# Kernel optimization log

Measured on AMD Instinct MI355X. Metric: run time of the kernel, lower is better.

Reference implementation:

```python
import jax, jax.numpy as jnp
import numpy as np

MAXHD = 100.0
MAXV = 40.0
LSTM_UNITS = 20
IN_DIM = 12


def setup_inputs() -> dict:
    key = jax.random.key(0)
    ks = jax.random.split(key, 10)
    nveh, nt = 8192, 512
    leadfol_inputs = jax.random.normal(ks[0], (nveh, nt, IN_DIM), dtype=jnp.float32)
    true_traj = jax.random.normal(ks[1], (nveh, nt), dtype=jnp.float32)
    hidden_states = jnp.zeros((2, nveh, LSTM_UNITS), dtype=jnp.float32)
    s = 0.1
    # LSTM kernel/recurrent kernel/bias (keras gate order: i, f, c, o)
    W_k = jax.random.normal(ks[2], (IN_DIM, 4 * LSTM_UNITS), dtype=jnp.float32) * s
    W_r = jax.random.normal(ks[3], (LSTM_UNITS, 4 * LSTM_UNITS), dtype=jnp.float32) * s
    b_l = jnp.zeros((4 * LSTM_UNITS,), dtype=jnp.float32)
    # dense (10, relu) and lc_actions (3)
    W_d = jax.random.normal(ks[4], (LSTM_UNITS, 10), dtype=jnp.float32) * s
    b_d = jnp.zeros((10,), dtype=jnp.float32)
    W_lc = jax.random.normal(ks[5], (10, 3), dtype=jnp.float32) * s
    b_lc = jnp.zeros((3,), dtype=jnp.float32)
    return {"leadfol_inputs": leadfol_inputs, "true_traj": true_traj,
            "hidden_states": hidden_states, "W_k": W_k, "W_r": W_r, "b_l": b_l,
            "W_d": W_d, "b_d": b_d, "W_lc": W_lc, "b_lc": b_lc}


def reference(leadfol_inputs, true_traj, hidden_states, W_k, W_r, b_l, W_d, b_d, W_lc, b_lc):
    # time-major for scan: (nt, nveh, ...)
    lf_t = jnp.swapaxes(leadfol_inputs, 0, 1)
    pos_t = jnp.swapaxes(true_traj, 0, 1)

    def step(carry, xt):
        h, c = carry
        pos, lf = xt  # pos: (nveh,), lf: (nveh, 12)
        lead_hd = (lf[:, :3] - pos[:, None]) / MAXHD
        fol_hd = (pos[:, None] - lf[:, 3:6]) / MAXHD
        spds = lf[:, 6:] / MAXV
        x = jnp.concatenate([lead_hd, fol_hd, spds], axis=1)
        x = jnp.where(jnp.isnan(x), jnp.ones_like(x), x)
        z = x @ W_k + h @ W_r + b_l
        zi, zf, zg, zo = jnp.split(z, 4, axis=1)
        c = jax.nn.sigmoid(zf) * c + jax.nn.sigmoid(zi) * jnp.tanh(zg)
        h = jax.nn.sigmoid(zo) * jnp.tanh(c)
        d = jax.nn.relu(h @ W_d + b_d)
        lc = d @ W_lc + b_lc
        return (h, c), lc

    (h, c), lc_t = jax.lax.scan(step, (hidden_states[0], hidden_states[1]), (pos_t, lf_t))
    pred_lc_action = jnp.swapaxes(lc_t, 0, 1)  # (nveh, nt, 3)
    return (true_traj, pred_lc_action, h, c)
```

## Files before the change

### kernel.cpp

```cpp
#include <hip/hip_runtime.h>

#define NVEH 8192
#define NT   512

typedef short bf16x8 __attribute__((ext_vector_type(8)));
typedef float f32x4  __attribute__((ext_vector_type(4)));

__device__ __forceinline__ float fsig(float x) {
    float e = __builtin_amdgcn_exp2f(-1.44269504f * x);
    return __builtin_amdgcn_rcpf(1.0f + e);
}
__device__ __forceinline__ float ftanh(float x) {
    float e = __builtin_amdgcn_exp2f(-2.88539008f * x);
    return 2.0f * __builtin_amdgcn_rcpf(1.0f + e) - 1.0f;
}
__device__ __forceinline__ unsigned short f2bf(float f) {
    union { float f; unsigned u; } v; v.f = f;
    unsigned r = v.u + 0x7fff + ((v.u >> 16) & 1);
    return (unsigned short)(r >> 16);
}

__global__ __launch_bounds__(64) void lstm_scan_kernel(
    const float* __restrict__ lead,
    const float* __restrict__ traj,
    const float* __restrict__ hidden,
    const float* __restrict__ W_k,
    const float* __restrict__ W_r,
    const float* __restrict__ b_l,
    const float* __restrict__ W_d,
    const float* __restrict__ b_d,
    const float* __restrict__ W_lc,
    const float* __restrict__ b_lc,
    float* __restrict__ out_lc,
    float* __restrict__ out_h,
    float* __restrict__ out_c)
{
    __shared__ alignas(16) unsigned short xhb[16 * 40];
    __shared__ alignas(16) unsigned short hb [16 * 40];
    __shared__ alignas(16) unsigned short db [16 * 40];

    const int lane = threadIdx.x;
    const int q    = lane >> 4;
    const int v    = lane & 15;
    const int gv   = blockIdx.x * 16 + v;

    for (int i = lane; i < 640; i += 64) { xhb[i] = 0; hb[i] = 0; db[i] = 0; }

    bf16x8 aW[5]; f32x4 cB[5];
    #pragma unroll
    for (int tt = 0; tt < 5; ++tt) {
        #pragma unroll
        for (int j = 0; j < 8; ++j) {
            int k = q * 8 + j;
            int p = 16 * tt + v;
            int u = p >> 2, g = p & 3;
            int col = g * 20 + u;
            float w = (k < 12) ? W_k[k * 80 + col] : W_r[(k - 12) * 80 + col];
            aW[tt][j] = (short)f2bf(w);
        }
        #pragma unroll
        for (int reg = 0; reg < 4; ++reg)
            cB[tt][reg] = b_l[reg * 20 + 4 * tt + q];
    }
    bf16x8 aH; f32x4 cD;
    #pragma unroll
    for (int j = 0; j < 8; ++j) {
        int k = q * 8 + j;
        aH[j] = (v < 10 && k < 20) ? (short)f2bf(W_d[k * 10 + v]) : (short)0;
    }
    #pragma unroll
    for (int reg = 0; reg < 4; ++reg) {
        int m = 4 * q + reg;
        cD[reg] = (m < 10) ? b_d[m] : 0.0f;
    }
    bf16x8 aL; f32x4 cL;
    #pragma unroll
    for (int j = 0; j < 8; ++j) {
        int k = q * 8 + j;
        aL[j] = (v < 3 && k < 10) ? (short)f2bf(W_lc[k * 3 + v]) : (short)0;
    }
    #pragma unroll
    for (int reg = 0; reg < 4; ++reg) {
        int m = 4 * q + reg;
        cL[reg] = (m < 3) ? b_lc[m] : 0.0f;
    }

    float cst[5], h32[5];
    #pragma unroll
    for (int tt = 0; tt < 5; ++tt) {
        int u = 4 * tt + q;
        h32[tt] = hidden[(size_t)gv * 20 + u];
        cst[tt] = hidden[(size_t)NVEH * 20 + (size_t)gv * 20 + u];
    }
    #pragma unroll
    for (int tt = 0; tt < 5; ++tt) {
        int u = 4 * tt + q;
        unsigned short hu = f2bf(h32[tt]);
        xhb[v * 40 + 12 + u] = hu;
    }

    float Ac[4], Bc[4];
    #pragma unroll
    for (int i = 0; i < 4; ++i) {
        int e = 4 * q + i;
        if (e < 3)      { Ac[i] =  0.01f;  Bc[i] = -0.01f; }
        else if (e < 6) { Ac[i] = -0.01f;  Bc[i] =  0.01f; }
        else            { Ac[i] =  0.025f; Bc[i] =  0.0f;  }
    }

    const float* lf = lead + (size_t)gv * NT * 12;
    const float* ps = traj + (size_t)gv * NT;
    float* lcout    = out_lc + (size_t)gv * NT * 3;

    float4 r0 = make_float4(0.f, 0.f, 0.f, 0.f);
    float  p0 = 0.f;
    if (q < 3) r0 = *(const float4*)(lf + q * 4);
    if (q < 2) p0 = ps[0];
    if (q < 3) {
        float xv[4] = { r0.x, r0.y, r0.z, r0.w };
        #pragma unroll
        for (int i = 0; i < 4; ++i) {
            float x = fmaf(xv[i], Ac[i], p0 * Bc[i]);
            xv[i] = (x == x) ? x : 1.0f;
        }
        uint2 val;
        val.x = (unsigned)f2bf(xv[0]) | ((unsigned)f2bf(xv[1]) << 16);
        val.y = (unsigned)f2bf(xv[2]) | ((unsigned)f2bf(xv[3]) << 16);
        *(uint2*)&xhb[v * 40 + q * 4] = val;
    }

    float4 rA = make_float4(0.f,0.f,0.f,0.f), rB = make_float4(0.f,0.f,0.f,0.f);
    float  pA = 0.f, pB = 0.f;
    if (q < 3) { rA = *(const float4*)(lf + 12 * 1 + q * 4);
                 rB = *(const float4*)(lf + 12 * 2 + q * 4); }
    if (q < 2) { pA = ps[1]; pB = ps[2]; }

    __syncthreads();

    for (int t = 0; t < NT; ++t) {
        bf16x8 bx = *(const bf16x8*)&xhb[v * 40 + q * 8];

        f32x4 z[5];
        #pragma unroll
        for (int tt = 0; tt < 5; ++tt)
            z[tt] = __builtin_amdgcn_mfma_f32_16x16x32_bf16(aW[tt], bx, cB[tt], 0, 0, 0);

        #pragma unroll
        for (int tt = 0; tt < 5; ++tt) {
            float si = fsig(z[tt][0]);
            float sf = fsig(z[tt][1]);
            float tg = ftanh(z[tt][2]);
            float so = fsig(z[tt][3]);
            float cn = fmaf(sf, cst[tt], si * tg);
            cst[tt] = cn;
            h32[tt] = so * ftanh(cn);
        }

        #pragma unroll
        for (int tt = 0; tt < 5; ++tt) {
            int u = 4 * tt + q;
            unsigned short hu = f2bf(h32[tt]);
            xhb[v * 40 + 12 + u] = hu;
            hb [v * 40 + u]      = hu;
        }
        __builtin_amdgcn_wave_barrier();

        bf16x8 bh = *(const bf16x8*)&hb[v * 40 + q * 8];
        f32x4 d = __builtin_amdgcn_mfma_f32_16x16x32_bf16(aH, bh, cD, 0, 0, 0);
        #pragma unroll
        for (int reg = 0; reg < 4; ++reg)
            db[v * 40 + 4 * q + reg] = f2bf(fmaxf(d[reg], 0.0f));
        __builtin_amdgcn_wave_barrier();

        bf16x8 bd2 = *(const bf16x8*)&db[v * 40 + q * 8];
        f32x4 lcv = __builtin_amdgcn_mfma_f32_16x16x32_bf16(aL, bd2, cL, 0, 0, 0);
        if (q == 0) {
            float* o = lcout + (size_t)t * 3;
            o[0] = lcv[0]; o[1] = lcv[1]; o[2] = lcv[2];
        }

        if (q < 3) {
            float xv[4] = { rA.x, rA.y, rA.z, rA.w };
            #pragma unroll
            for (int i = 0; i < 4; ++i) {
                float x = fmaf(xv[i], Ac[i], pA * Bc[i]);
                xv[i] = (x == x) ? x : 1.0f;
            }
            uint2 val;
            val.x = (unsigned)f2bf(xv[0]) | ((unsigned)f2bf(xv[1]) << 16);
            val.y = (unsigned)f2bf(xv[2]) | ((unsigned)f2bf(xv[3]) << 16);
            *(uint2*)&xhb[v * 40 + q * 4] = val;
        }

        rA = rB; pA = pB;
        int tn = (t + 3 < NT) ? (t + 3) : (NT - 1);
        if (q < 3) rB = *(const float4*)(lf + 12 * tn + q * 4);
        if (q < 2) pB = ps[tn];
        __builtin_amdgcn_wave_barrier();
    }

    #pragma unroll
    for (int tt = 0; tt < 5; ++tt) {
        int u = 4 * tt + q;
        out_h[(size_t)gv * 20 + u] = h32[tt];
        out_c[(size_t)gv * 20 + u] = cst[tt];
    }
}

extern "C" void kernel_launch(void* const* d_in, const int* in_sizes, int n_in,
                              void* d_out, int out_size, void* d_ws, size_t ws_size,
                              hipStream_t stream) {
    const float* lead   = (const float*)d_in[0];
    const float* traj   = (const float*)d_in[1];
    const float* hidden = (const float*)d_in[2];
    const float* W_k    = (const float*)d_in[3];
    const float* W_r    = (const float*)d_in[4];
    const float* b_l    = (const float*)d_in[5];
    const float* W_d    = (const float*)d_in[6];
    const float* b_d    = (const float*)d_in[7];
    const float* W_lc   = (const float*)d_in[8];
    const float* b_lc   = (const float*)d_in[9];

    float* out    = (float*)d_out;
    float* out_tt = out;
    float* out_lc = out + (size_t)NVEH * NT;
    float* out_h  = out_lc + (size_t)NVEH * NT * 3;
    float* out_c  = out_h + (size_t)NVEH * 20;

    hipMemcpyAsync(out_tt, traj, (size_t)NVEH * NT * sizeof(float),
                   hipMemcpyDeviceToDevice, stream);

    lstm_scan_kernel<<<dim3(NVEH / 16), dim3(64), 0, stream>>>(
        lead, traj, hidden, W_k, W_r, b_l, W_d, b_d, W_lc, b_lc,
        out_lc, out_h, out_c);
}
```

Before: 816.4 us.

## Build LSTM input operand in registers and fuse the dense/lc head

Replaces the three LDS staging buffers with one h-row buffer. The next step's combined [x,h] MFMA operand is now assembled from register shuffles plus a single LDS read. The dense layer reuses that combined operand, with its weights shifted to the h rows, and the 10x3 lc projection becomes per-lane FMAs plus xor-shuffle reductions instead of a third MFMA and another LDS round trip. The aim is to shorten the serial per-timestep dependency chain. In exchange it adds shuffle traffic, rotates which lane group writes the output, and uses float2 stores that can be unaligned on odd timesteps.

```diff
diff --git a/kernel.cpp b/kernel.cpp
--- a/kernel.cpp
+++ b/kernel.cpp
@@ -15,36 +15,26 @@
     return 2.0f * __builtin_amdgcn_rcpf(1.0f + e) - 1.0f;
 }
 __device__ __forceinline__ unsigned short f2bf(float f) {
-    union { float f; unsigned u; } v; v.f = f;
-    unsigned r = v.u + 0x7fff + ((v.u >> 16) & 1);
+    union { float f; unsigned u; } vv; vv.f = f;
+    unsigned r = vv.u + 0x7fff + ((vv.u >> 16) & 1);
     return (unsigned short)(r >> 16);
 }
 
 __global__ __launch_bounds__(64) void lstm_scan_kernel(
-    const float* __restrict__ lead,
-    const float* __restrict__ traj,
+    const float* __restrict__ lead, const float* __restrict__ traj,
     const float* __restrict__ hidden,
-    const float* __restrict__ W_k,
-    const float* __restrict__ W_r,
-    const float* __restrict__ b_l,
-    const float* __restrict__ W_d,
-    const float* __restrict__ b_d,
-    const float* __restrict__ W_lc,
+    const float* __restrict__ W_k, const float* __restrict__ W_r,
+    const float* __restrict__ b_l, const float* __restrict__ W_d,
+    const float* __restrict__ b_d, const float* __restrict__ W_lc,
     const float* __restrict__ b_lc,
-    float* __restrict__ out_lc,
-    float* __restrict__ out_h,
-    float* __restrict__ out_c)
+    float* __restrict__ out_lc, float* __restrict__ out_h, float* __restrict__ out_c)
 {
-    __shared__ alignas(16) unsigned short xhb[16 * 40];
-    __shared__ alignas(16) unsigned short hb [16 * 40];
-    __shared__ alignas(16) unsigned short db [16 * 40];
+    __shared__ alignas(16) unsigned short hrow[16 * 40];
 
     const int lane = threadIdx.x;
     const int q    = lane >> 4;
     const int v    = lane & 15;
     const int gv   = blockIdx.x * 16 + v;
-
-    for (int i = lane; i < 640; i += 64) { xhb[i] = 0; hb[i] = 0; db[i] = 0; }
 
     bf16x8 aW[5]; f32x4 cB[5];
     #pragma unroll
@@ -66,26 +56,24 @@
     #pragma unroll
     for (int j = 0; j < 8; ++j) {
         int k = q * 8 + j;
-        aH[j] = (v < 10 && k < 20) ? (short)f2bf(W_d[k * 10 + v]) : (short)0;
+        aH[j] = (v < 10 && k >= 12) ? (short)f2bf(W_d[(k - 12) * 10 + v]) : (short)0;
     }
     #pragma unroll
     for (int reg = 0; reg < 4; ++reg) {
         int m = 4 * q + reg;
         cD[reg] = (m < 10) ? b_d[m] : 0.0f;
     }
-    bf16x8 aL; f32x4 cL;
-    #pragma unroll
-    for (int j = 0; j < 8; ++j) {
-        int k = q * 8 + j;
-        aL[j] = (v < 3 && k < 10) ? (short)f2bf(W_lc[k * 3 + v]) : (short)0;
-    }
+    float wlc[4][3]; float pb0[3];
     #pragma unroll
     for (int reg = 0; reg < 4; ++reg) {
         int m = 4 * q + reg;
-        cL[reg] = (m < 3) ? b_lc[m] : 0.0f;
-    }
-
-    float cst[5], h32[5];
+        #pragma unroll
+        for (int j = 0; j < 3; ++j) wlc[reg][j] = (m < 10) ? W_lc[m * 3 + j] : 0.0f;
+    }
+    #pragma unroll
+    for (int j = 0; j < 3; ++j) pb0[j] = (q == 0) ? b_lc[j] : 0.0f;
+
+    float h32[5], cst[5];
     #pragma unroll
     for (int tt = 0; tt < 5; ++tt) {
         int u = 4 * tt + q;
@@ -95,8 +83,8 @@
     #pragma unroll
     for (int tt = 0; tt < 5; ++tt) {
         int u = 4 * tt + q;
-        unsigned short hu = f2bf(h32[tt]);
-        xhb[v * 40 + 12 + u] = hu;
+        int idx = (tt == 0) ? u : u + 4;
+        hrow[v * 40 + idx] = f2bf(h32[tt]);
     }
 
     float Ac[4], Bc[4];
@@ -112,34 +100,43 @@
     const float* ps = traj + (size_t)gv * NT;
     float* lcout    = out_lc + (size_t)gv * NT * 3;
 
-    float4 r0 = make_float4(0.f, 0.f, 0.f, 0.f);
-    float  p0 = 0.f;
+    float4 r0 = make_float4(0.f,0.f,0.f,0.f); float p0s = 0.f;
     if (q < 3) r0 = *(const float4*)(lf + q * 4);
-    if (q < 2) p0 = ps[0];
+    if (q < 2) p0s = ps[0];
+    unsigned pk0 = 0, pk1 = 0;
     if (q < 3) {
         float xv[4] = { r0.x, r0.y, r0.z, r0.w };
         #pragma unroll
         for (int i = 0; i < 4; ++i) {
-            float x = fmaf(xv[i], Ac[i], p0 * Bc[i]);
+            float x = fmaf(xv[i], Ac[i], p0s * Bc[i]);
             xv[i] = (x == x) ? x : 1.0f;
         }
-        uint2 val;
-        val.x = (unsigned)f2bf(xv[0]) | ((unsigned)f2bf(xv[1]) << 16);
-        val.y = (unsigned)f2bf(xv[2]) | ((unsigned)f2bf(xv[3]) << 16);
-        *(uint2*)&xhb[v * 40 + q * 4] = val;
+        pk0 = (unsigned)f2bf(xv[0]) | ((unsigned)f2bf(xv[1]) << 16);
+        pk1 = (unsigned)f2bf(xv[2]) | ((unsigned)f2bf(xv[3]) << 16);
+    }
+    __builtin_amdgcn_wave_barrier();
+
+    bf16x8 bx;
+    {
+        unsigned s0 = __shfl_down(pk0, 16), s1 = __shfl_down(pk1, 16);
+        uint2 hA = make_uint2(0, 0); uint4 hB = make_uint4(0, 0, 0, 0);
+        if (q == 1) hA = *(const uint2*)&hrow[v * 40];
+        if (q >= 2) hB = *(const uint4*)&hrow[v * 40 + (q == 2 ? 8 : 16)];
+        unsigned dw0 = (q == 0) ? pk0 : (q == 1) ? s0   : hB.x;
+        unsigned dw1 = (q == 0) ? pk1 : (q == 1) ? s1   : hB.y;
+        unsigned dw2 = (q == 0) ? s0  : (q == 1) ? hA.x : hB.z;
+        unsigned dw3 = (q == 0) ? s1  : (q == 1) ? hA.y : hB.w;
+        uint4 tmp = make_uint4(dw0, dw1, dw2, dw3);
+        bx = *(bf16x8*)&tmp;
     }
 
     float4 rA = make_float4(0.f,0.f,0.f,0.f), rB = make_float4(0.f,0.f,0.f,0.f);
-    float  pA = 0.f, pB = 0.f;
+    float pA = 0.f, pB = 0.f;
     if (q < 3) { rA = *(const float4*)(lf + 12 * 1 + q * 4);
                  rB = *(const float4*)(lf + 12 * 2 + q * 4); }
     if (q < 2) { pA = ps[1]; pB = ps[2]; }
 
-    __syncthreads();
-
     for (int t = 0; t < NT; ++t) {
-        bf16x8 bx = *(const bf16x8*)&xhb[v * 40 + q * 8];
-
         f32x4 z[5];
         #pragma unroll
         for (int tt = 0; tt < 5; ++tt)
@@ -159,24 +156,8 @@
         #pragma unroll
         for (int tt = 0; tt < 5; ++tt) {
             int u = 4 * tt + q;
-            unsigned short hu = f2bf(h32[tt]);
-            xhb[v * 40 + 12 + u] = hu;
-            hb [v * 40 + u]      = hu;
-        }
-        __builtin_amdgcn_wave_barrier();
-
-        bf16x8 bh = *(const bf16x8*)&hb[v * 40 + q * 8];
-        f32x4 d = __builtin_amdgcn_mfma_f32_16x16x32_bf16(aH, bh, cD, 0, 0, 0);
-        #pragma unroll
-        for (int reg = 0; reg < 4; ++reg)
-            db[v * 40 + 4 * q + reg] = f2bf(fmaxf(d[reg], 0.0f));
-        __builtin_amdgcn_wave_barrier();
-
-        bf16x8 bd2 = *(const bf16x8*)&db[v * 40 + q * 8];
-        f32x4 lcv = __builtin_amdgcn_mfma_f32_16x16x32_bf16(aL, bd2, cL, 0, 0, 0);
-        if (q == 0) {
-            float* o = lcout + (size_t)t * 3;
-            o[0] = lcv[0]; o[1] = lcv[1]; o[2] = lcv[2];
+            int idx = (tt == 0) ? u : u + 4;
+            hrow[v * 40 + idx] = f2bf(h32[tt]);
         }
 
         if (q < 3) {
@@ -186,11 +167,48 @@
                 float x = fmaf(xv[i], Ac[i], pA * Bc[i]);
                 xv[i] = (x == x) ? x : 1.0f;
             }
-            uint2 val;
-            val.x = (unsigned)f2bf(xv[0]) | ((unsigned)f2bf(xv[1]) << 16);
-            val.y = (unsigned)f2bf(xv[2]) | ((unsigned)f2bf(xv[3]) << 16);
-            *(uint2*)&xhb[v * 40 + q * 4] = val;
-        }
+            pk0 = (unsigned)f2bf(xv[0]) | ((unsigned)f2bf(xv[1]) << 16);
+            pk1 = (unsigned)f2bf(xv[2]) | ((unsigned)f2bf(xv[3]) << 16);
+        }
+        __builtin_amdgcn_wave_barrier();
+
+        bf16x8 bxn;
+        {
+            unsigned s0 = __shfl_down(pk0, 16), s1 = __shfl_down(pk1, 16);
+            uint2 hA = make_uint2(0, 0); uint4 hB = make_uint4(0, 0, 0, 0);
+            if (q == 1) hA = *(const uint2*)&hrow[v * 40];
+            if (q >= 2) hB = *(const uint4*)&hrow[v * 40 + (q == 2 ? 8 : 16)];
+            unsigned dw0 = (q == 0) ? pk0 : (q == 1) ? s0   : hB.x;
+            unsigned dw1 = (q == 0) ? pk1 : (q == 1) ? s1   : hB.y;
+            unsigned dw2 = (q == 0) ? s0  : (q == 1) ? hA.x : hB.z;
+            unsigned dw3 = (q == 0) ? s1  : (q == 1) ? hA.y : hB.w;
+            uint4 tmp = make_uint4(dw0, dw1, dw2, dw3);
+            bxn = *(bf16x8*)&tmp;
+        }
+
+        f32x4 d = __builtin_amdgcn_mfma_f32_16x16x32_bf16(aH, bxn, cD, 0, 0, 0);
+        float dr[4];
+        #pragma unroll
+        for (int reg = 0; reg < 4; ++reg) dr[reg] = fmaxf(d[reg], 0.0f);
+
+        float p[3];
+        #pragma unroll
+        for (int j = 0; j < 3; ++j) {
+            float acc = pb0[j];
+            #pragma unroll
+            for (int reg = 0; reg < 4; ++reg) acc = fmaf(dr[reg], wlc[reg][j], acc);
+            acc += __shfl_xor(acc, 16);
+            acc += __shfl_xor(acc, 32);
+            p[j] = acc;
+        }
+
+        if (q == (t & 3)) {
+            float* o = lcout + (size_t)t * 3;
+            *(float2*)o = make_float2(p[0], p[1]);
+            o[2] = p[2];
+        }
+
+        bx = bxn;
 
         rA = rB; pA = pB;
         int tn = (t + 3 < NT) ? (t + 3) : (NT - 1);
```

New measurement: 797.6 us. -2.3%, faster.
